# Performance work log

Measured on AMD Instinct MI355X. Metric: run time of the kernel, lower is better.

## Reference

```python
import jax, jax.numpy as jnp
import numpy as np

N_GRIDS = 16
N_FEATS = 2
GRID_SHAPE = (64, 64, 64)  # D, H, W
NODES = 64
N_OUT = 1
DATA_MIN = 0.0
DATA_MAX = 1.0
N_POINTS = 524288


def setup_inputs() -> dict:
    key = jax.random.key(0)
    ks = jax.random.split(key, 12)
    x = jax.random.uniform(ks[0], (N_POINTS, 3), jnp.float32, -1.0, 1.0)
    # matches randomize_grids(): scales ~ log(1 - U*0.05), rotations ~ identity quat + noise,
    # translations ~ U(-0.05, 0.05)
    scales = jnp.log(1.0 - jax.random.uniform(ks[1], (N_GRIDS, 3), jnp.float32) * 0.05)
    rotations = jnp.zeros((N_GRIDS, 4), jnp.float32).at[:, 3].set(1.0) \
        + jax.random.normal(ks[2], (N_GRIDS, 4), jnp.float32) * 0.05
    translations = jax.random.uniform(ks[3], (N_GRIDS, 3), jnp.float32) * 0.1 - 0.05
    # original uses U(-1e-4, 1e-4); use a larger scale for numerically meaningful outputs
    feature_grids = jax.random.uniform(ks[4], (N_GRIDS, N_FEATS) + GRID_SHAPE,
                                       jnp.float32, -0.1, 0.1)
    d_in = N_GRIDS * N_FEATS
    def xavier(k, fi, fo):
        std = np.sqrt(2.0 / (fi + fo)).astype(np.float32)
        return jax.random.normal(k, (fi, fo), jnp.float32) * std
    W0 = xavier(ks[5], d_in, NODES)
    b0 = jax.random.normal(ks[6], (NODES,), jnp.float32) * 0.001
    W1 = xavier(ks[7], NODES, NODES)
    b1 = jax.random.normal(ks[8], (NODES,), jnp.float32) * 0.001
    W2 = xavier(ks[9], NODES, N_OUT)
    b2 = jax.random.normal(ks[10], (N_OUT,), jnp.float32) * 0.001
    return {"x": x, "rotations": rotations, "scales": scales,
            "translations": translations, "feature_grids": feature_grids,
            "W0": W0, "b0": b0, "W1": W1, "b1": b1, "W2": W2, "b2": b2}


def quat_to_rot(q):
    # q: [G,4] in (x, y, z, w) order; normalized (rotation_activation)
    q = q / jnp.linalg.norm(q, axis=-1, keepdims=True)
    x, y, z, w = q[:, 0], q[:, 1], q[:, 2], q[:, 3]
    r0 = jnp.stack([1 - 2 * (y * y + z * z), 2 * (x * y - z * w), 2 * (x * z + y * w)], -1)
    r1 = jnp.stack([2 * (x * y + z * w), 1 - 2 * (x * x + z * z), 2 * (y * z - x * w)], -1)
    r2 = jnp.stack([2 * (x * z - y * w), 2 * (y * z + x * w), 1 - 2 * (x * x + y * y)], -1)
    return jnp.stack([r0, r1, r2], axis=-2)  # [G,3,3]


def transform_points(x, rotations, scales, translations):
    # S*R*T order: local = diag(exp(scales)) @ R @ x + t, per grid -> [G,N,3]
    R = quat_to_rot(rotations)
    s = jnp.exp(scales)
    M = s[:, :, None] * R  # [G,3,3]
    return jnp.einsum('gij,nj->gni', M, x) + translations[:, None, :]


def trilinear_sample(grid, pts):
    # grid: [C,D,H,W]; pts: [N,3] (x,y,z) in [-1,1]; grid_sample semantics:
    # mode='bilinear', align_corners=True, padding_mode='zeros'
    C, D, H, W = grid.shape
    fx = (pts[:, 0] + 1.0) * 0.5 * (W - 1)
    fy = (pts[:, 1] + 1.0) * 0.5 * (H - 1)
    fz = (pts[:, 2] + 1.0) * 0.5 * (D - 1)
    x0 = jnp.floor(fx); y0 = jnp.floor(fy); z0 = jnp.floor(fz)
    wx = fx - x0; wy = fy - y0; wz = fz - z0
    x0i = x0.astype(jnp.int32); y0i = y0.astype(jnp.int32); z0i = z0.astype(jnp.int32)

    def corner(dx, dy, dz):
        xi = x0i + dx; yi = y0i + dy; zi = z0i + dz
        valid = (xi >= 0) & (xi < W) & (yi >= 0) & (yi < H) & (zi >= 0) & (zi < D)
        v = grid[:, jnp.clip(zi, 0, D - 1), jnp.clip(yi, 0, H - 1), jnp.clip(xi, 0, W - 1)]
        w = ((wx if dx else 1 - wx) * (wy if dy else 1 - wy) * (wz if dz else 1 - wz))
        return v * jnp.where(valid, w, 0.0)[None, :]

    out = corner(0, 0, 0)
    for dz in (0, 1):
        for dy in (0, 1):
            for dx in (0, 1):
                if (dx, dy, dz) != (0, 0, 0):
                    out = out + corner(dx, dy, dz)
    return out  # [C,N]


def reference(x, rotations, scales, translations, feature_grids, W0, b0, W1, b1, W2, b2):
    pts = transform_points(x, rotations, scales, translations)      # [G,N,3]
    feats = jax.vmap(trilinear_sample)(feature_grids, pts)          # [G,C,N]
    feats = feats.transpose(2, 0, 1).reshape(x.shape[0], -1)        # [N, G*C]
    h = jax.nn.relu(feats @ W0 + b0)
    h = jax.nn.relu(h @ W1 + b1)
    y = h @ W2 + b2
    return y * (DATA_MAX - DATA_MIN) + DATA_MIN
```

## Files before the change

kernel.cpp:

```cpp
#include <hip/hip_runtime.h>
#include <cstddef>
#include <cstdint>

constexpr int NPTS   = 524288;
constexpr int NG     = 16;
constexpr int GR     = 64;
constexpr int GR3    = GR * GR * GR;
constexpr int NNODES = 64;
constexpr int NBINS  = 32768;

constexpr size_t GRIDS_BYTES = (size_t)NG * GR3 * 8;
constexpr size_t WS_SORT     = GRIDS_BYTES;
constexpr size_t SORT_BYTES  = (size_t)NPTS * 16;
constexpr size_t WS_KEYR     = WS_SORT + SORT_BYTES;
constexpr size_t KEYR_BYTES  = (size_t)NPTS * 4;
constexpr size_t WS_BINS     = WS_KEYR + KEYR_BYTES;
constexpr size_t BINS_BYTES  = (size_t)NBINS * 4;
constexpr size_t WS_MATS     = WS_BINS + BINS_BYTES;
constexpr size_t MATS_BYTES  = 1024;
constexpr size_t WS_WPACK    = WS_MATS + MATS_BYTES;
constexpr size_t WPACK_BYTES = (size_t)(256 + 512) * 16;
constexpr size_t WS_PART     = WS_WPACK + WPACK_BYTES;
constexpr size_t PART_BYTES  = 128 * 4;
constexpr size_t WS_TOTAL    = WS_PART + PART_BYTES;

constexpr int PREP_REPACK = 4096;
constexpr int PREP_HIST   = 2048;

typedef _Float16 half8 __attribute__((ext_vector_type(8)));
typedef float    floatx4 __attribute__((ext_vector_type(4)));

__device__ __forceinline__ unsigned part1by2(unsigned x) {
    x &= 0x3ff;
    x = (x | (x << 16)) & 0x030000FF;
    x = (x | (x <<  8)) & 0x0300F00F;
    x = (x | (x <<  4)) & 0x030C30C3;
    x = (x | (x <<  2)) & 0x09249249;
    return x;
}

__device__ __forceinline__ unsigned cell_of(float px, float py, float pz) {
    int cx = (int)((px + 1.0f) * 16.0f); cx = min(max(cx, 0), 31);
    int cy = (int)((py + 1.0f) * 16.0f); cy = min(max(cy, 0), 31);
    int cz = (int)((pz + 1.0f) * 16.0f); cz = min(max(cz, 0), 31);
    return part1by2((unsigned)cx) | (part1by2((unsigned)cy) << 1) | (part1by2((unsigned)cz) << 2);
}

__device__ __forceinline__ unsigned f32_to_bf16_rne(float f) {
    unsigned u = __float_as_uint(f);
    return (u + 0x7fffu + ((u >> 16) & 1u)) >> 16;
}

__device__ __forceinline__ unsigned pack_h2(float a, float b) {
    unsigned short ua = __builtin_bit_cast(unsigned short, (_Float16)a);
    unsigned short ub = __builtin_bit_cast(unsigned short, (_Float16)b);
    return (unsigned)ua | ((unsigned)ub << 16);
}

__device__ __forceinline__ unsigned short f32_to_h16(float a) {
    return __builtin_bit_cast(unsigned short, (_Float16)a);
}

__global__ __launch_bounds__(256) void prep_kernel(
    const float* __restrict__ grids, uint2* __restrict__ gout,
    const float* __restrict__ xs, unsigned* __restrict__ bins,
    unsigned* __restrict__ keyrank,
    const float* __restrict__ rot, const float* __restrict__ scl,
    const float* __restrict__ trn, float* __restrict__ mats,
    const float* __restrict__ W0, const float* __restrict__ W1,
    uint4* __restrict__ wpack)
{
    const int bid = blockIdx.x;
    const int tid = threadIdx.x;

    if (bid < PREP_REPACK) {
        const int base = (bid * 256 + tid) * 4;
        const int g    = base >> 18;
        const int node = base & (GR3 - 1);
        const int x    = node & 63;
        const float* p0 = grids + (size_t)g * 2 * GR3 + node;
        const float* p1 = p0 + GR3;
        const float4 c0 = *(const float4*)p0;
        const float4 c1 = *(const float4*)p1;
        float d0n, d1n;
        if (x == 60) { d0n = c0.w; d1n = c1.w; }
        else         { d0n = p0[4]; d1n = p1[4]; }
        const float e0[5] = {c0.x, c0.y, c0.z, c0.w, d0n};
        const float e1[5] = {c1.x, c1.y, c1.z, c1.w, d1n};
        unsigned pk[5];
        #pragma unroll
        for (int i = 0; i < 5; ++i)
            pk[i] = f32_to_bf16_rne(e0[i]) | (f32_to_bf16_rne(e1[i]) << 16);
        uint4* dst = (uint4*)(gout + (size_t)g * GR3 + node);
        dst[0] = make_uint4(pk[0], pk[1], pk[1], pk[2]);
        dst[1] = make_uint4(pk[2], pk[3], pk[3], pk[4]);
    } else if (bid < PREP_REPACK + PREP_HIST) {
        const int n = (bid - PREP_REPACK) * 256 + tid;
        const unsigned key = cell_of(xs[n*3+0], xs[n*3+1], xs[n*3+2]);
        const unsigned rank = atomicAdd(&bins[key], 1u);
        keyrank[n] = key | (rank << 15);
    } else if (bid == PREP_REPACK + PREP_HIST) {
        const int g = tid;
        if (g < NG) {
            float qx = rot[g*4+0], qy = rot[g*4+1], qz = rot[g*4+2], qw = rot[g*4+3];
            const float inv = 1.0f / sqrtf(qx*qx + qy*qy + qz*qz + qw*qw);
            qx *= inv; qy *= inv; qz *= inv; qw *= inv;
            const float sx = expf(scl[g*3+0]);
            const float sy = expf(scl[g*3+1]);
            const float sz = expf(scl[g*3+2]);
            float* m = mats + g * 12;
            m[0] = sx * (1.0f - 2.0f*(qy*qy + qz*qz));
            m[1] = sx * (2.0f*(qx*qy - qz*qw));
            m[2] = sx * (2.0f*(qx*qz + qy*qw));
            m[3] = sy * (2.0f*(qx*qy + qz*qw));
            m[4] = sy * (1.0f - 2.0f*(qx*qx + qz*qz));
            m[5] = sy * (2.0f*(qy*qz - qx*qw));
            m[6] = sz * (2.0f*(qx*qz - qy*qw));
            m[7] = sz * (2.0f*(qy*qz + qx*qw));
            m[8] = sz * (1.0f - 2.0f*(qx*qx + qy*qy));
            m[9]  = trn[g*3+0];
            m[10] = trn[g*3+1];
            m[11] = trn[g*3+2];
        }
    } else {
        const int t = tid >> 6;
        const int lane = tid & 63;
        const int q = lane >> 4, c = lane & 15;
        const int n = t * 16 + c;
        {
            unsigned u[4];
            #pragma unroll
            for (int jj = 0; jj < 4; ++jj) {
                const int k0 = q * 8 + 2 * jj;
                u[jj] = pack_h2(W0[k0 * NNODES + n], W0[(k0 + 1) * NNODES + n]);
            }
            wpack[t * 64 + lane] = make_uint4(u[0], u[1], u[2], u[3]);
        }
        #pragma unroll
        for (int ks = 0; ks < 2; ++ks) {
            unsigned u[4];
            #pragma unroll
            for (int jj = 0; jj < 4; ++jj) {
                const int k0 = ks * 32 + q * 8 + 2 * jj;
                u[jj] = pack_h2(W1[k0 * NNODES + n], W1[(k0 + 1) * NNODES + n]);
            }
            wpack[256 + (ks * 4 + t) * 64 + lane] = make_uint4(u[0], u[1], u[2], u[3]);
        }
    }
}

__global__ __launch_bounds__(256) void scanA_kernel(unsigned* __restrict__ bins,
                                                    unsigned* __restrict__ part) {
    __shared__ unsigned s[256];
    const int t = threadIdx.x;
    const int base = blockIdx.x * 256;
    const unsigned v = bins[base + t];
    s[t] = v;
    __syncthreads();
    for (int off = 1; off < 256; off <<= 1) {
        unsigned u = (t >= off) ? s[t - off] : 0u;
        __syncthreads();
        s[t] += u;
        __syncthreads();
    }
    bins[base + t] = s[t] - v;
    if (t == 255) part[blockIdx.x] = s[255];
}

__global__ __launch_bounds__(128) void scanB_kernel(unsigned* __restrict__ part) {
    __shared__ unsigned s[128];
    const int t = threadIdx.x;
    const unsigned v = part[t];
    s[t] = v;
    __syncthreads();
    for (int off = 1; off < 128; off <<= 1) {
        unsigned u = (t >= off) ? s[t - off] : 0u;
        __syncthreads();
        s[t] += u;
        __syncthreads();
    }
    part[t] = s[t] - v;
}

__global__ __launch_bounds__(256) void scatter_kernel(const float* __restrict__ xs,
                                                      const unsigned* __restrict__ bins,
                                                      const unsigned* __restrict__ part,
                                                      const unsigned* __restrict__ keyrank,
                                                      float4* __restrict__ sorted) {
    const int n = blockIdx.x * 256 + threadIdx.x;
    if (n >= NPTS) return;
    const unsigned kr = keyrank[n];
    const unsigned key = kr & 0x7fffu;
    const unsigned rank = kr >> 15;
    const unsigned pos = part[key >> 8] + bins[key] + rank;
    sorted[pos] = make_float4(xs[n*3+0], xs[n*3+1], xs[n*3+2], __int_as_float(n));
}

struct Geom {
    int i00, i01, i10, i11;
    float ax0, ax1, ay0, ay1, az0, az1;
    unsigned selhi, sello;
};

__device__ __forceinline__ Geom make_geom(const float* __restrict__ m,
                                          float px, float py, float pz, int g) {
    Geom G;
    const float tx = fmaf(m[0], px, fmaf(m[1], py, fmaf(m[2], pz, m[9])));
    const float ty = fmaf(m[3], px, fmaf(m[4], py, fmaf(m[5], pz, m[10])));
    const float tz = fmaf(m[6], px, fmaf(m[7], py, fmaf(m[8], pz, m[11])));
    const float fx = (tx + 1.0f) * 31.5f;
    const float fy = (ty + 1.0f) * 31.5f;
    const float fz = (tz + 1.0f) * 31.5f;
    const float x0f = floorf(fx), y0f = floorf(fy), z0f = floorf(fz);
    const float wx = fx - x0f, wy = fy - y0f, wz = fz - z0f;
    const int x0 = (int)x0f, y0 = (int)y0f, z0 = (int)z0f;
    G.ax0 = ((unsigned)x0       < 64u) ? (1.0f - wx) : 0.0f;
    G.ax1 = ((unsigned)(x0 + 1) < 64u) ? wx          : 0.0f;
    G.ay0 = ((unsigned)y0       < 64u) ? (1.0f - wy) : 0.0f;
    G.ay1 = ((unsigned)(y0 + 1) < 64u) ? wy          : 0.0f;
    G.az0 = ((unsigned)z0       < 64u) ? (1.0f - wz) : 0.0f;
    G.az1 = ((unsigned)(z0 + 1) < 64u) ? wz          : 0.0f;
    G.selhi = (x0 >= 63) ? 1u : 0u;
    G.sello = (x0 <= -1) ? 1u : 0u;
    const int xb  = min(max(x0, 0), 62);
    const int yc0 = min(max(y0, 0), 63),     yc1 = min(max(y0 + 1, 0), 63);
    const int zc0 = min(max(z0, 0), 63),     zc1 = min(max(z0 + 1, 0), 63);
    const int b = (g << 18) + xb;
    G.i00 = b + (zc0 << 12) + (yc0 << 6);
    G.i01 = b + (zc0 << 12) + (yc1 << 6);
    G.i10 = b + (zc1 << 12) + (yc0 << 6);
    G.i11 = b + (zc1 << 12) + (yc1 << 6);
    return G;
}

__device__ __forceinline__ void acc_pair(float& f0, float& f1, const Geom& G,
                                         uint2 q, float wyz) {
    const unsigned v0 = G.selhi ? q.y : q.x;
    const unsigned v1 = G.sello ? q.x : q.y;
    float s0 = G.ax0 * __uint_as_float(v0 << 16);
    s0 = fmaf(G.ax1, __uint_as_float(v1 << 16), s0);
    f0 = fmaf(wyz, s0, f0);
    float s1 = G.ax0 * __uint_as_float(v0 & 0xffff0000u);
    s1 = fmaf(G.ax1, __uint_as_float(v1 & 0xffff0000u), s1);
    f1 = fmaf(wyz, s1, f1);
}

constexpr int HSTR    = 72;
constexpr int ARENA_H = 64 * HSTR;
constexpr int FSTRIDE = 40;

__global__ __launch_bounds__(256, 4) void amgsrn_main(
    const float4* __restrict__ sorted,
    const uint2*  __restrict__ gridsP,
    const float*  __restrict__ mats,
    const uint4*  __restrict__ wpack,
    const float*  __restrict__ b0,
    const float*  __restrict__ b1,
    const float*  __restrict__ W2,
    const float*  __restrict__ b2,
    float* __restrict__ out)
{
    __shared__ unsigned short sh[4 * ARENA_H];
    __shared__ float yS[256];

    const int tid  = threadIdx.x;
    const int lane = tid & 63;
    const int wv   = tid >> 6;
    const int c    = lane & 15;
    const int q    = lane >> 4;
    unsigned short* wa = sh + wv * ARENA_H;

    const int n = blockIdx.x * 256 + tid;
    const float4 p = sorted[n];
    const float px = p.x, py = p.y, pz = p.z;
    const int orig = __float_as_int(p.w);

    unsigned pk[NG];
    Geom Ga = make_geom(mats, px, py, pz, 0);
    uint2 a00 = gridsP[Ga.i00], a01 = gridsP[Ga.i01];
    uint2 a10 = gridsP[Ga.i10], a11 = gridsP[Ga.i11];
    Geom Gb = make_geom(mats + 12, px, py, pz, 1);
    uint2 b00 = gridsP[Gb.i00], b01 = gridsP[Gb.i01];
    uint2 b10 = gridsP[Gb.i10], b11 = gridsP[Gb.i11];
    #pragma unroll
    for (int g = 0; g < NG; ++g) {
        Geom Gn;
        uint2 n00, n01, n10, n11;
        if (g + 2 < NG) {
            Gn = make_geom(mats + (g + 2) * 12, px, py, pz, g + 2);
            n00 = gridsP[Gn.i00]; n01 = gridsP[Gn.i01];
            n10 = gridsP[Gn.i10]; n11 = gridsP[Gn.i11];
        }
        float f0 = 0.0f, f1 = 0.0f;
        acc_pair(f0, f1, Ga, a00, Ga.az0 * Ga.ay0);
        acc_pair(f0, f1, Ga, a01, Ga.az0 * Ga.ay1);
        acc_pair(f0, f1, Ga, a10, Ga.az1 * Ga.ay0);
        acc_pair(f0, f1, Ga, a11, Ga.az1 * Ga.ay1);
        pk[g] = pack_h2(f0, f1);
        Ga = Gb; a00 = b00; a01 = b01; a10 = b10; a11 = b11;
        if (g + 2 < NG) {
            Gb = Gn; b00 = n00; b01 = n01; b10 = n10; b11 = n11;
        }
    }

    {
        uint4* dst = (uint4*)(wa + lane * FSTRIDE);
        dst[0] = make_uint4(pk[0],  pk[1],  pk[2],  pk[3]);
        dst[1] = make_uint4(pk[4],  pk[5],  pk[6],  pk[7]);
        dst[2] = make_uint4(pk[8],  pk[9],  pk[10], pk[11]);
        dst[3] = make_uint4(pk[12], pk[13], pk[14], pk[15]);
    }
    __syncthreads();

    half8 a0[4];
    #pragma unroll
    for (int m = 0; m < 4; ++m)
        a0[m] = *(const half8*)(wa + (m * 16 + c) * FSTRIDE + q * 8);

    half8 b0f[4], b1f[2][4];
    #pragma unroll
    for (int t = 0; t < 4; ++t)
        b0f[t] = __builtin_bit_cast(half8, wpack[t * 64 + lane]);
    #pragma unroll
    for (int ks = 0; ks < 2; ++ks)
        #pragma unroll
        for (int t = 0; t < 4; ++t)
            b1f[ks][t] = __builtin_bit_cast(half8, wpack[256 + (ks * 4 + t) * 64 + lane]);
    float b0v[4], b1v[4], w2v[4];
    #pragma unroll
    for (int t = 0; t < 4; ++t) {
        b0v[t] = b0[t * 16 + c];
        b1v[t] = b1[t * 16 + c];
        w2v[t] = W2[t * 16 + c];
    }
    const float b2s = b2[0];

    __syncthreads();

    #pragma unroll
    for (int t = 0; t < 4; ++t) {
        #pragma unroll
        for (int m = 0; m < 4; ++m) {
            floatx4 acc = {b0v[t], b0v[t], b0v[t], b0v[t]};
            acc = __builtin_amdgcn_mfma_f32_16x16x32_f16(a0[m], b0f[t], acc, 0, 0, 0);
            const int node = t * 16 + c;
            const int ptb  = m * 16 + q * 4;
            #pragma unroll
            for (int r = 0; r < 4; ++r)
                wa[(ptb + r) * HSTR + node] = f32_to_h16(fmaxf(acc[r], 0.0f));
        }
    }
    __syncthreads();

    half8 a1[4][2];
    #pragma unroll
    for (int m = 0; m < 4; ++m)
        #pragma unroll
        for (int ks = 0; ks < 2; ++ks)
            a1[m][ks] = *(const half8*)(wa + (m * 16 + c) * HSTR + ks * 32 + q * 8);

    float p4[4][4];
    #pragma unroll
    for (int m = 0; m < 4; ++m)
        #pragma unroll
        for (int r = 0; r < 4; ++r) p4[m][r] = 0.0f;

    #pragma unroll
    for (int t = 0; t < 4; ++t) {
        #pragma unroll
        for (int m = 0; m < 4; ++m) {
            floatx4 acc = {b1v[t], b1v[t], b1v[t], b1v[t]};
            acc = __builtin_amdgcn_mfma_f32_16x16x32_f16(a1[m][0], b1f[0][t], acc, 0, 0, 0);
            acc = __builtin_amdgcn_mfma_f32_16x16x32_f16(a1[m][1], b1f[1][t], acc, 0, 0, 0);
            #pragma unroll
            for (int r = 0; r < 4; ++r)
                p4[m][r] = fmaf(fmaxf(acc[r], 0.0f), w2v[t], p4[m][r]);
        }
    }

    #pragma unroll
    for (int m = 0; m < 4; ++m)
        #pragma unroll
        for (int r = 0; r < 4; ++r) {
            float v = p4[m][r];
            v += __shfl_xor(v, 1, 64);
            v += __shfl_xor(v, 2, 64);
            v += __shfl_xor(v, 4, 64);
            v += __shfl_xor(v, 8, 64);
            p4[m][r] = v + b2s;
        }

    if (c == 0) {
        #pragma unroll
        for (int m = 0; m < 4; ++m)
            #pragma unroll
            for (int r = 0; r < 4; ++r)
                yS[wv * 64 + m * 16 + q * 4 + r] = p4[m][r];
    }
    __syncthreads();
    out[orig] = yS[tid];
}

__global__ __launch_bounds__(256, 3) void amgsrn_fused_fallback(
    const float* __restrict__ xs,
    const float* __restrict__ rot,
    const float* __restrict__ scl,
    const float* __restrict__ trn,
    const float* __restrict__ grids,
    const float* __restrict__ W0,
    const float* __restrict__ b0,
    const float* __restrict__ W1,
    const float* __restrict__ b1,
    const float* __restrict__ W2,
    const float* __restrict__ b2,
    float* __restrict__ out)
{
    __shared__ float sM[NG][12];
    const int tid = threadIdx.x;
    if (tid < NG) {
        const int g = tid;
        float qx = rot[g*4+0], qy = rot[g*4+1], qz = rot[g*4+2], qw = rot[g*4+3];
        const float inv = 1.0f / sqrtf(qx*qx + qy*qy + qz*qz + qw*qw);
        qx *= inv; qy *= inv; qz *= inv; qw *= inv;
        const float sx = expf(scl[g*3+0]);
        const float sy = expf(scl[g*3+1]);
        const float sz = expf(scl[g*3+2]);
        sM[g][0] = sx * (1.0f - 2.0f*(qy*qy + qz*qz));
        sM[g][1] = sx * (2.0f*(qx*qy - qz*qw));
        sM[g][2] = sx * (2.0f*(qx*qz + qy*qw));
        sM[g][3] = sy * (2.0f*(qx*qy + qz*qw));
        sM[g][4] = sy * (1.0f - 2.0f*(qx*qx + qz*qz));
        sM[g][5] = sy * (2.0f*(qy*qz - qx*qw));
        sM[g][6] = sz * (2.0f*(qx*qz - qy*qw));
        sM[g][7] = sz * (2.0f*(qy*qz + qx*qw));
        sM[g][8] = sz * (1.0f - 2.0f*(qx*qx + qy*qy));
        sM[g][9]  = trn[g*3+0];
        sM[g][10] = trn[g*3+1];
        sM[g][11] = trn[g*3+2];
    }
    __syncthreads();

    const int n = blockIdx.x * blockDim.x + tid;
    if (n >= NPTS) return;
    const float px = xs[n*3+0];
    const float py = xs[n*3+1];
    const float pz = xs[n*3+2];

    float h0[NNODES];
    #pragma unroll
    for (int j = 0; j < NNODES; ++j) h0[j] = b0[j];

    #pragma unroll
    for (int g = 0; g < NG; ++g) {
        const float* m = sM[g];
        const float tx = m[0]*px + m[1]*py + m[2]*pz + m[9];
        const float ty = m[3]*px + m[4]*py + m[5]*pz + m[10];
        const float tz = m[6]*px + m[7]*py + m[8]*pz + m[11];
        const float fx = (tx + 1.0f) * 31.5f;
        const float fy = (ty + 1.0f) * 31.5f;
        const float fz = (tz + 1.0f) * 31.5f;
        const float x0f = floorf(fx), y0f = floorf(fy), z0f = floorf(fz);
        const float wx = fx - x0f, wy = fy - y0f, wz = fz - z0f;
        const int x0 = (int)x0f, y0 = (int)y0f, z0 = (int)z0f;
        const float* gb = grids + (size_t)g * (size_t)(2 * GR3);
        float f0 = 0.0f, f1 = 0.0f;
        #pragma unroll
        for (int dz = 0; dz < 2; ++dz) {
            #pragma unroll
            for (int dy = 0; dy < 2; ++dy) {
                #pragma unroll
                for (int dx = 0; dx < 2; ++dx) {
                    const int xi = x0 + dx, yi = y0 + dy, zi = z0 + dz;
                    const bool valid = ((unsigned)xi < (unsigned)GR) &
                                       ((unsigned)yi < (unsigned)GR) &
                                       ((unsigned)zi < (unsigned)GR);
                    const int xc = min(max(xi, 0), GR-1);
                    const int yc = min(max(yi, 0), GR-1);
                    const int zc = min(max(zi, 0), GR-1);
                    float w = (dx ? wx : 1.0f - wx) *
                              (dy ? wy : 1.0f - wy) *
                              (dz ? wz : 1.0f - wz);
                    w = valid ? w : 0.0f;
                    const int idx = (zc * GR + yc) * GR + xc;
                    f0 = fmaf(w, gb[idx], f0);
                    f1 = fmaf(w, gb[idx + GR3], f1);
                }
            }
        }
        const float* w0a = W0 + (2*g    ) * NNODES;
        const float* w0b = W0 + (2*g + 1) * NNODES;
        #pragma unroll
        for (int j = 0; j < NNODES; ++j)
            h0[j] = fmaf(f1, w0b[j], fmaf(f0, w0a[j], h0[j]));
    }
    #pragma unroll
    for (int j = 0; j < NNODES; ++j) h0[j] = fmaxf(h0[j], 0.0f);

    float y = b2[0];
    #pragma unroll
    for (int half = 0; half < 2; ++half) {
        float h1[32];
        #pragma unroll
        for (int j = 0; j < 32; ++j) h1[j] = b1[half * 32 + j];
        #pragma unroll
        for (int k = 0; k < NNODES; ++k) {
            const float a = h0[k];
            const float* w = W1 + k * NNODES + half * 32;
            #pragma unroll
            for (int j = 0; j < 32; ++j) h1[j] = fmaf(a, w[j], h1[j]);
        }
        #pragma unroll
        for (int j = 0; j < 32; ++j) y = fmaf(fmaxf(h1[j], 0.0f), W2[half * 32 + j], y);
    }

    out[n] = y;
}

extern "C" void kernel_launch(void* const* d_in, const int* in_sizes, int n_in,
                              void* d_out, int out_size, void* d_ws, size_t ws_size,
                              hipStream_t stream) {
    const float* xs  = (const float*)d_in[0];
    const float* rot = (const float*)d_in[1];
    const float* scl = (const float*)d_in[2];
    const float* trn = (const float*)d_in[3];
    const float* gr  = (const float*)d_in[4];
    const float* W0  = (const float*)d_in[5];
    const float* b0  = (const float*)d_in[6];
    const float* W1  = (const float*)d_in[7];
    const float* b1  = (const float*)d_in[8];
    const float* W2  = (const float*)d_in[9];
    const float* b2  = (const float*)d_in[10];
    float* out = (float*)d_out;

    if (ws_size < WS_TOTAL) {
        dim3 grid((NPTS + 255) / 256), block(256);
        hipLaunchKernelGGL(amgsrn_fused_fallback, grid, block, 0, stream,
                           xs, rot, scl, trn, gr, W0, b0, W1, b1, W2, b2, out);
        return;
    }

    char* ws = (char*)d_ws;
    uint2*    gridsP  = (uint2*)(ws);
    float4*   sorted  = (float4*)(ws + WS_SORT);
    unsigned* keyrank = (unsigned*)(ws + WS_KEYR);
    unsigned* bins    = (unsigned*)(ws + WS_BINS);
    float*    mats    = (float*)(ws + WS_MATS);
    uint4*    wpack   = (uint4*)(ws + WS_WPACK);
    unsigned* part    = (unsigned*)(ws + WS_PART);

    hipMemsetAsync(bins, 0, BINS_BYTES, stream);
    hipLaunchKernelGGL(prep_kernel, dim3(PREP_REPACK + PREP_HIST + 2), dim3(256), 0, stream,
                       gr, gridsP, xs, bins, keyrank,
                       rot, scl, trn, mats, W0, W1, wpack);
    hipLaunchKernelGGL(scanA_kernel, dim3(NBINS / 256), dim3(256), 0, stream, bins, part);
    hipLaunchKernelGGL(scanB_kernel, dim3(1), dim3(128), 0, stream, part);
    hipLaunchKernelGGL(scatter_kernel, dim3(NPTS / 256), dim3(256), 0, stream,
                       xs, bins, part, keyrank, sorted);
    hipLaunchKernelGGL(amgsrn_main, dim3(NPTS / 256), dim3(256), 0, stream,
                       sorted, gridsP, mats, wpack, b0, b1, W2, b2, out);
}
```

Before: 189.2 us.

## Swizzle LDS arena, drop x-edge selects, shuffle outputs directly, raise occupancy

Replaces the padded LDS layouts (strides 40/72) with a 64-wide XOR-swizzled layout, which shrinks shared memory per wave. It also removes the yS buffer and final barrier by scattering outputs through wave shuffles, and raises launch bounds from 4 to 5 waves per SIMD. The x-boundary handling now folds the select logic into the weights, with index clamps up to 63. This may read one element past an x-row at x0=63, which relies on the packed grid layout holding the adjacent element. Output stores become 16 predicated scattered writes per lane group instead of one coalesced store per thread.

```diff
diff --git a/kernel.cpp b/kernel.cpp
--- a/kernel.cpp
+++ b/kernel.cpp
@@ -197,9 +197,8 @@
 }
 
 struct Geom {
-    int i00, i01, i10, i11;
+    unsigned i00, i01, i10, i11;
     float ax0, ax1, ay0, ay1, az0, az1;
-    unsigned selhi, sello;
 };
 
 __device__ __forceinline__ Geom make_geom(const float* __restrict__ m,
@@ -214,42 +213,43 @@
     const float x0f = floorf(fx), y0f = floorf(fy), z0f = floorf(fz);
     const float wx = fx - x0f, wy = fy - y0f, wz = fz - z0f;
     const int x0 = (int)x0f, y0 = (int)y0f, z0 = (int)z0f;
-    G.ax0 = ((unsigned)x0       < 64u) ? (1.0f - wx) : 0.0f;
-    G.ax1 = ((unsigned)(x0 + 1) < 64u) ? wx          : 0.0f;
+    float ax0 = ((unsigned)x0       < 64u) ? (1.0f - wx) : 0.0f;
+    float ax1 = ((unsigned)(x0 + 1) < 64u) ? wx          : 0.0f;
+    const bool wrap = (x0 == -1);
+    G.ax0 = wrap ? ax1 : ax0;
+    G.ax1 = wrap ? 0.0f : ax1;
     G.ay0 = ((unsigned)y0       < 64u) ? (1.0f - wy) : 0.0f;
     G.ay1 = ((unsigned)(y0 + 1) < 64u) ? wy          : 0.0f;
     G.az0 = ((unsigned)z0       < 64u) ? (1.0f - wz) : 0.0f;
     G.az1 = ((unsigned)(z0 + 1) < 64u) ? wz          : 0.0f;
-    G.selhi = (x0 >= 63) ? 1u : 0u;
-    G.sello = (x0 <= -1) ? 1u : 0u;
-    const int xb  = min(max(x0, 0), 62);
+    const int xb  = min(max(x0, 0), 63);
     const int yc0 = min(max(y0, 0), 63),     yc1 = min(max(y0 + 1, 0), 63);
     const int zc0 = min(max(z0, 0), 63),     zc1 = min(max(z0 + 1, 0), 63);
-    const int b = (g << 18) + xb;
-    G.i00 = b + (zc0 << 12) + (yc0 << 6);
-    G.i01 = b + (zc0 << 12) + (yc1 << 6);
-    G.i10 = b + (zc1 << 12) + (yc0 << 6);
-    G.i11 = b + (zc1 << 12) + (yc1 << 6);
+    const unsigned b = (unsigned)(g << 18) + (unsigned)xb;
+    G.i00 = b + (unsigned)((zc0 << 12) + (yc0 << 6));
+    G.i01 = b + (unsigned)((zc0 << 12) + (yc1 << 6));
+    G.i10 = b + (unsigned)((zc1 << 12) + (yc0 << 6));
+    G.i11 = b + (unsigned)((zc1 << 12) + (yc1 << 6));
     return G;
 }
 
 __device__ __forceinline__ void acc_pair(float& f0, float& f1, const Geom& G,
                                          uint2 q, float wyz) {
-    const unsigned v0 = G.selhi ? q.y : q.x;
-    const unsigned v1 = G.sello ? q.x : q.y;
-    float s0 = G.ax0 * __uint_as_float(v0 << 16);
-    s0 = fmaf(G.ax1, __uint_as_float(v1 << 16), s0);
+    float s0 = G.ax0 * __uint_as_float(q.x << 16);
+    s0 = fmaf(G.ax1, __uint_as_float(q.y << 16), s0);
     f0 = fmaf(wyz, s0, f0);
-    float s1 = G.ax0 * __uint_as_float(v0 & 0xffff0000u);
-    s1 = fmaf(G.ax1, __uint_as_float(v1 & 0xffff0000u), s1);
+    float s1 = G.ax0 * __uint_as_float(q.x & 0xffff0000u);
+    s1 = fmaf(G.ax1, __uint_as_float(q.y & 0xffff0000u), s1);
     f1 = fmaf(wyz, s1, f1);
 }
 
-constexpr int HSTR    = 72;
-constexpr int ARENA_H = 64 * HSTR;
-constexpr int FSTRIDE = 40;
-
-__global__ __launch_bounds__(256, 4) void amgsrn_main(
+constexpr int ARENA_H = 64 * 64;
+
+__device__ __forceinline__ int sw_addr(int row, int halfcol) {
+    return row * 64 + ((((halfcol >> 3) ^ (row & 7)) << 3) | (halfcol & 7));
+}
+
+__global__ __launch_bounds__(256, 5) void amgsrn_main(
     const float4* __restrict__ sorted,
     const uint2*  __restrict__ gridsP,
     const float*  __restrict__ mats,
@@ -261,7 +261,6 @@
     float* __restrict__ out)
 {
     __shared__ unsigned short sh[4 * ARENA_H];
-    __shared__ float yS[256];
 
     const int tid  = threadIdx.x;
     const int lane = tid & 63;
@@ -303,19 +302,16 @@
         }
     }
 
-    {
-        uint4* dst = (uint4*)(wa + lane * FSTRIDE);
-        dst[0] = make_uint4(pk[0],  pk[1],  pk[2],  pk[3]);
-        dst[1] = make_uint4(pk[4],  pk[5],  pk[6],  pk[7]);
-        dst[2] = make_uint4(pk[8],  pk[9],  pk[10], pk[11]);
-        dst[3] = make_uint4(pk[12], pk[13], pk[14], pk[15]);
-    }
+    #pragma unroll
+    for (int g4 = 0; g4 < 4; ++g4)
+        *(uint4*)(wa + sw_addr(lane, g4 * 8)) =
+            make_uint4(pk[g4*4+0], pk[g4*4+1], pk[g4*4+2], pk[g4*4+3]);
     __syncthreads();
 
     half8 a0[4];
     #pragma unroll
     for (int m = 0; m < 4; ++m)
-        a0[m] = *(const half8*)(wa + (m * 16 + c) * FSTRIDE + q * 8);
+        a0[m] = *(const half8*)(wa + sw_addr(m * 16 + c, q * 8));
 
     half8 b0f[4], b1f[2][4];
     #pragma unroll
@@ -347,7 +343,7 @@
             const int ptb  = m * 16 + q * 4;
             #pragma unroll
             for (int r = 0; r < 4; ++r)
-                wa[(ptb + r) * HSTR + node] = f32_to_h16(fmaxf(acc[r], 0.0f));
+                wa[sw_addr(ptb + r, node)] = f32_to_h16(fmaxf(acc[r], 0.0f));
         }
     }
     __syncthreads();
@@ -357,7 +353,7 @@
     for (int m = 0; m < 4; ++m)
         #pragma unroll
         for (int ks = 0; ks < 2; ++ks)
-            a1[m][ks] = *(const half8*)(wa + (m * 16 + c) * HSTR + ks * 32 + q * 8);
+            a1[m][ks] = *(const half8*)(wa + sw_addr(m * 16 + c, ks * 32 + q * 8));
 
     float p4[4][4];
     #pragma unroll
@@ -390,15 +386,14 @@
             p4[m][r] = v + b2s;
         }
 
-    if (c == 0) {
-        #pragma unroll
-        for (int m = 0; m < 4; ++m)
-            #pragma unroll
-            for (int r = 0; r < 4; ++r)
-                yS[wv * 64 + m * 16 + q * 4 + r] = p4[m][r];
-    }
-    __syncthreads();
-    out[orig] = yS[tid];
+    #pragma unroll
+    for (int m = 0; m < 4; ++m)
+        #pragma unroll
+        for (int r = 0; r < 4; ++r) {
+            const int srcPt = m * 16 + q * 4 + r;
+            const int origPt = __shfl(orig, srcPt, 64);
+            if (c == 0) out[origPt] = p4[m][r];
+        }
 }
 
 __global__ __launch_bounds__(256, 3) void amgsrn_fused_fallback(
```

Result: slower. 206.2 us (+9.0%).
